# Kernel tuning notes

Measured on AMD Instinct MI355X. Metric: run time of the kernel, lower is better.

## Reference

```python
import jax, jax.numpy as jnp
import numpy as np

QMAX = 32767.0   # 2**15 - 1
QMIN = -32768.0  # -2**15


def setup_inputs() -> dict:
    key = jax.random.key(0)
    k_x, k_w0, k_w1, k_s, k_b = jax.random.split(key, 5)
    N, Cin, Cout = 8192, 4096, 4096
    x = jax.random.normal(k_x, (N, Cin, 1, 1), dtype=jnp.float32)
    # Fake-quantized INT8 weights: build a fp32 weight, split into dual int8 planes
    # the same way prepare_from_weight does, so w0/w1 hold integer values in [-128,127].
    W = jax.random.normal(k_w0, (Cout, Cin), dtype=jnp.float32) * 0.02
    max_abs = jnp.maximum(jnp.max(jnp.abs(W), axis=1), 1e-8)
    s0 = max_abs / 127.0
    w0 = jnp.clip(jnp.round(W / s0[:, None]), -128.0, 127.0)
    R = W - s0[:, None] * w0
    max_abs_R = jnp.max(jnp.abs(R), axis=1)
    s1 = jnp.where(max_abs_R > 1e-3, max_abs_R / 127.0, 0.0)
    w1 = jnp.where((s1 > 0)[:, None],
                   jnp.clip(jnp.round(R / jnp.where(s1 > 0, s1, 1.0)[:, None]), -128.0, 127.0),
                   0.0)
    bias = jax.random.normal(k_b, (Cout,), dtype=jnp.float32) * 0.01
    return {"x": x, "w0": w0, "w1": w1, "s0": s0, "s1": s1, "bias": bias}


def reference(x, w0, w1, s0, s1, bias):
    N, Cin, H, W_ = x.shape  # H == W_ == 1
    x2d = x.reshape(N, Cin)
    # INT16 activation fake-quant with softplus-smoothed amax
    amax = jnp.max(jnp.abs(x2d), axis=1, keepdims=True)          # [N,1]
    scale_x = jax.nn.softplus(amax) / QMAX                       # [N,1]
    xq = jnp.clip(jnp.round(x2d / scale_x), QMIN, QMAX)          # [N,Cin]
    # dual 1x1 convs == two GEMMs: [N,Cin] x [Cin,Cout]
    y0 = jnp.einsum('nc,oc->no', xq, w0)
    y1 = jnp.einsum('nc,oc->no', xq, w1)
    y = (y0 * s0[None, :] + y1 * s1[None, :]) * scale_x + bias[None, :]
    return y.reshape(N, -1, 1, 1)
```

## Files before the change

### kernel.cpp

```cpp
#include <hip/hip_runtime.h>
#include <hip/hip_fp16.h>

#define N_ROWS 8192
#define K_DIM  4096
#define M_DIM  4096

typedef __attribute__((ext_vector_type(8))) _Float16 half8;
typedef __attribute__((ext_vector_type(4))) _Float16 half4v;
typedef __attribute__((ext_vector_type(4))) float    f32x4;

__global__ __launch_bounds__(256) void prologue_kernel(
    const float* __restrict__ x,  _Float16* __restrict__ xq, float* __restrict__ sx,
    const float* __restrict__ w0, const float* __restrict__ w1,
    const float* __restrict__ s0, const float* __restrict__ s1,
    _Float16* __restrict__ wp)
{
    const int t = threadIdx.x;
    if (blockIdx.x < N_ROWS) {
        const int row = blockIdx.x;
        const float4* xr4 = (const float4*)(x + (size_t)row * K_DIM);

        float4 v[4];
        float am = 0.0f;
#pragma unroll
        for (int i = 0; i < 4; ++i) {
            v[i] = xr4[i * 256 + t];
            am = fmaxf(am, fmaxf(fmaxf(fabsf(v[i].x), fabsf(v[i].y)),
                                 fmaxf(fabsf(v[i].z), fabsf(v[i].w))));
        }
#pragma unroll
        for (int off = 32; off; off >>= 1)
            am = fmaxf(am, __shfl_xor(am, off, 64));
        __shared__ float red[4];
        if ((t & 63) == 0) red[t >> 6] = am;
        __syncthreads();
        am = fmaxf(fmaxf(red[0], red[1]), fmaxf(red[2], red[3]));

        const float sp    = (am > 20.0f) ? am : log1pf(expf(am));
        const float scale = sp / 32767.0f;
        const float inv   = 32767.0f / sp;
        if (t == 0) sx[row] = scale;

        half4v* out4 = (half4v*)(xq + (size_t)row * K_DIM);
#pragma unroll
        for (int i = 0; i < 4; ++i) {
            float q0 = fminf(fmaxf(rintf(v[i].x * inv), -32768.0f), 32767.0f);
            float q1 = fminf(fmaxf(rintf(v[i].y * inv), -32768.0f), 32767.0f);
            float q2 = fminf(fmaxf(rintf(v[i].z * inv), -32768.0f), 32767.0f);
            float q3 = fminf(fmaxf(rintf(v[i].w * inv), -32768.0f), 32767.0f);
            half4v h;
            h[0] = (_Float16)q0; h[1] = (_Float16)q1;
            h[2] = (_Float16)q2; h[3] = (_Float16)q3;
            out4[i * 256 + t] = h;
        }
    } else {
        const size_t gid  = (size_t)(blockIdx.x - N_ROWS) * 256 + t;
        const size_t base = gid * 8;
        const int    o    = (int)(base >> 12);
        const float  a = s0[o], b = s1[o];

        const float4* p0 = (const float4*)(w0 + base);
        const float4* p1 = (const float4*)(w1 + base);
        float4 u0 = p0[0], u1 = p0[1];
        float4 v0 = p1[0], v1 = p1[1];

        half8 h;
        h[0] = (_Float16)(a * u0.x + b * v0.x);
        h[1] = (_Float16)(a * u0.y + b * v0.y);
        h[2] = (_Float16)(a * u0.z + b * v0.z);
        h[3] = (_Float16)(a * u0.w + b * v0.w);
        h[4] = (_Float16)(a * u1.x + b * v1.x);
        h[5] = (_Float16)(a * u1.y + b * v1.y);
        h[6] = (_Float16)(a * u1.z + b * v1.z);
        h[7] = (_Float16)(a * u1.w + b * v1.w);
        *(half8*)(wp + base) = h;
    }
}

__device__ inline void async_load16(const void* g, void* l)
{
    __builtin_amdgcn_global_load_lds(
        (const __attribute__((address_space(1))) void*)g,
        (__attribute__((address_space(3))) void*)l, 16, 0, 0);
}

__global__ __launch_bounds__(256) void gemm_kernel(
    const _Float16* __restrict__ A,
    const _Float16* __restrict__ B,
    const float* __restrict__ sx,
    const float* __restrict__ bias,
    float* __restrict__ out)
{
    __shared__ __align__(16) _Float16 As[128 * 32];
    __shared__ __align__(16) _Float16 Bs[128 * 32];

    const int t    = threadIdx.x;
    const int wave = t >> 6;
    const int lane = t & 63;

    const int tile = blockIdx.x >> 6;
    const int loc  = blockIdx.x & 63;
    const int o0   = ((tile & 3) * 8 + (loc & 7)) * 128;
    const int n0   = ((tile >> 2) * 8 + (loc >> 3)) * 128;

    const int srow = lane >> 2;
    const int scl  = lane & 3;
    const int scg  = scl ^ ((srow >> 1) & 3);
    const int gcol = scg * 8;
    const int lcol = scl * 8;

    const int n_off = (wave >> 1) * 64;
    const int o_off = (wave & 1) * 64;

    const int fr = lane & 15;
    const int fg = lane >> 4;
    const int fk = (fg ^ ((fr >> 1) & 3)) * 8;

    f32x4 acc[4][4] = {};

    for (int kk = 0; kk < K_DIM; kk += 32) {
#pragma unroll
        for (int j = 0; j < 2; ++j) {
            const int row = j * 64 + wave * 16 + srow;
            async_load16(A + (size_t)(n0 + row) * K_DIM + kk + gcol,
                         &As[row * 32 + lcol]);
            async_load16(B + (size_t)(o0 + row) * K_DIM + kk + gcol,
                         &Bs[row * 32 + lcol]);
        }
        __syncthreads();

        half8 af[4], bf[4];
#pragma unroll
        for (int i = 0; i < 4; ++i)
            af[i] = *(const half8*)&As[(n_off + i * 16 + fr) * 32 + fk];
#pragma unroll
        for (int j = 0; j < 4; ++j)
            bf[j] = *(const half8*)&Bs[(o_off + j * 16 + fr) * 32 + fk];

#pragma unroll
        for (int i = 0; i < 4; ++i)
#pragma unroll
            for (int j = 0; j < 4; ++j)
                acc[i][j] = __builtin_amdgcn_mfma_f32_16x16x32_f16(
                    af[i], bf[j], acc[i][j], 0, 0, 0);

        __syncthreads();
    }

#pragma unroll
    for (int i = 0; i < 4; ++i) {
        const int nbase = n0 + n_off + i * 16 + (lane >> 4) * 4;
#pragma unroll
        for (int r = 0; r < 4; ++r) {
            const float s = sx[nbase + r];
            float* orow = out + (size_t)(nbase + r) * M_DIM;
#pragma unroll
            for (int j = 0; j < 4; ++j) {
                const int o = o0 + o_off + j * 16 + (lane & 15);
                orow[o] = acc[i][j][r] * s + bias[o];
            }
        }
    }
}

extern "C" void kernel_launch(void* const* d_in, const int* in_sizes, int n_in,
                              void* d_out, int out_size, void* d_ws, size_t ws_size,
                              hipStream_t stream)
{
    const float* x    = (const float*)d_in[0];
    const float* w0   = (const float*)d_in[1];
    const float* w1   = (const float*)d_in[2];
    const float* s0   = (const float*)d_in[3];
    const float* s1   = (const float*)d_in[4];
    const float* bias = (const float*)d_in[5];
    float* out = (float*)d_out;

    char* ws = (char*)d_ws;
    _Float16* xq = (_Float16*)ws;
    _Float16* wp = (_Float16*)(ws + (size_t)N_ROWS * K_DIM * 2);
    float*    sx = (float*)(ws + (size_t)N_ROWS * K_DIM * 2
                               + (size_t)M_DIM * K_DIM * 2);

    prologue_kernel<<<N_ROWS + (M_DIM * K_DIM) / (256 * 8), 256, 0, stream>>>(
        x, xq, sx, w0, w1, s0, s1, wp);

    gemm_kernel<<<(N_ROWS / 128) * (M_DIM / 128), 256, 0, stream>>>(
        xq, wp, sx, bias, out);
}
```

Measured before the change: 638.8 us.

## Rewrite GEMM as 256x256 double-buffered pipelined kernel with wave-per-row prologue

The GEMM moves from 128x128 tiles with K=32 steps and a full sync per step to 256x256 tiles with 512 threads and K=64 double-buffered LDS stages. Async global-to-LDS loads are issued per quarter-phase, interleaved with MFMA work, and gated by explicit vmcnt waits and s_setprio. The block order is swizzled for L2 reuse and bias is loaded once into registers. The prologue now processes one activation row per wave, removing the LDS reduction and block barrier, and handles 16 weights per thread. This targets load latency and barrier stalls, at the cost of much higher register and LDS pressure (128 KB LDS per block) and delicate wait-count correctness.

Result: faster. 605.7 us (-5.2%).

```diff
diff --git a/kernel.cpp b/kernel.cpp
--- a/kernel.cpp
+++ b/kernel.cpp
@@ -4,6 +4,8 @@
 #define N_ROWS 8192
 #define K_DIM  4096
 #define M_DIM  4096
+#define NT     (K_DIM / 64)
+#define HT_MAX (4 * NT)
 
 typedef __attribute__((ext_vector_type(8))) _Float16 half8;
 typedef __attribute__((ext_vector_type(4))) _Float16 half4v;
@@ -16,64 +18,63 @@
     _Float16* __restrict__ wp)
 {
     const int t = threadIdx.x;
-    if (blockIdx.x < N_ROWS) {
-        const int row = blockIdx.x;
+    if (blockIdx.x < N_ROWS / 4) {
+        const int lane = t & 63;
+        const int row  = blockIdx.x * 4 + (t >> 6);
         const float4* xr4 = (const float4*)(x + (size_t)row * K_DIM);
 
-        float4 v[4];
+        float4 v[16];
         float am = 0.0f;
 #pragma unroll
-        for (int i = 0; i < 4; ++i) {
-            v[i] = xr4[i * 256 + t];
-            am = fmaxf(am, fmaxf(fmaxf(fabsf(v[i].x), fabsf(v[i].y)),
-                                 fmaxf(fabsf(v[i].z), fabsf(v[i].w))));
+        for (int j = 0; j < 16; ++j) {
+            v[j] = xr4[j * 64 + lane];
+            am = fmaxf(am, fmaxf(fmaxf(fabsf(v[j].x), fabsf(v[j].y)),
+                                 fmaxf(fabsf(v[j].z), fabsf(v[j].w))));
         }
 #pragma unroll
         for (int off = 32; off; off >>= 1)
             am = fmaxf(am, __shfl_xor(am, off, 64));
-        __shared__ float red[4];
-        if ((t & 63) == 0) red[t >> 6] = am;
-        __syncthreads();
-        am = fmaxf(fmaxf(red[0], red[1]), fmaxf(red[2], red[3]));
 
         const float sp    = (am > 20.0f) ? am : log1pf(expf(am));
-        const float scale = sp / 32767.0f;
+        const float scale = sp * (1.0f / 32767.0f);
         const float inv   = 32767.0f / sp;
-        if (t == 0) sx[row] = scale;
+        if (lane == 0) sx[row] = scale;
 
         half4v* out4 = (half4v*)(xq + (size_t)row * K_DIM);
 #pragma unroll
-        for (int i = 0; i < 4; ++i) {
-            float q0 = fminf(fmaxf(rintf(v[i].x * inv), -32768.0f), 32767.0f);
-            float q1 = fminf(fmaxf(rintf(v[i].y * inv), -32768.0f), 32767.0f);
-            float q2 = fminf(fmaxf(rintf(v[i].z * inv), -32768.0f), 32767.0f);
-            float q3 = fminf(fmaxf(rintf(v[i].w * inv), -32768.0f), 32767.0f);
+        for (int j = 0; j < 16; ++j) {
             half4v h;
-            h[0] = (_Float16)q0; h[1] = (_Float16)q1;
-            h[2] = (_Float16)q2; h[3] = (_Float16)q3;
-            out4[i * 256 + t] = h;
+            h[0] = (_Float16)fminf(fmaxf(rintf(v[j].x * inv), -32768.0f), 32767.0f);
+            h[1] = (_Float16)fminf(fmaxf(rintf(v[j].y * inv), -32768.0f), 32767.0f);
+            h[2] = (_Float16)fminf(fmaxf(rintf(v[j].z * inv), -32768.0f), 32767.0f);
+            h[3] = (_Float16)fminf(fmaxf(rintf(v[j].w * inv), -32768.0f), 32767.0f);
+            out4[j * 64 + lane] = h;
         }
     } else {
-        const size_t gid  = (size_t)(blockIdx.x - N_ROWS) * 256 + t;
-        const size_t base = gid * 8;
+        const size_t gid  = (size_t)(blockIdx.x - N_ROWS / 4) * 256 + t;
+        const size_t base = gid * 16;
         const int    o    = (int)(base >> 12);
         const float  a = s0[o], b = s1[o];
 
         const float4* p0 = (const float4*)(w0 + base);
         const float4* p1 = (const float4*)(w1 + base);
-        float4 u0 = p0[0], u1 = p0[1];
-        float4 v0 = p1[0], v1 = p1[1];
-
-        half8 h;
-        h[0] = (_Float16)(a * u0.x + b * v0.x);
-        h[1] = (_Float16)(a * u0.y + b * v0.y);
-        h[2] = (_Float16)(a * u0.z + b * v0.z);
-        h[3] = (_Float16)(a * u0.w + b * v0.w);
-        h[4] = (_Float16)(a * u1.x + b * v1.x);
-        h[5] = (_Float16)(a * u1.y + b * v1.y);
-        h[6] = (_Float16)(a * u1.z + b * v1.z);
-        h[7] = (_Float16)(a * u1.w + b * v1.w);
-        *(half8*)(wp + base) = h;
+        float4 u[4], w[4];
+#pragma unroll
+        for (int j = 0; j < 4; ++j) { u[j] = p0[j]; w[j] = p1[j]; }
+
+#pragma unroll
+        for (int hv = 0; hv < 2; ++hv) {
+            half8 h;
+#pragma unroll
+            for (int j = 0; j < 2; ++j) {
+                const float4 uu = u[hv * 2 + j], ww = w[hv * 2 + j];
+                h[j * 4 + 0] = (_Float16)(a * uu.x + b * ww.x);
+                h[j * 4 + 1] = (_Float16)(a * uu.y + b * ww.y);
+                h[j * 4 + 2] = (_Float16)(a * uu.z + b * ww.z);
+                h[j * 4 + 3] = (_Float16)(a * uu.w + b * ww.w);
+            }
+            *(half8*)(wp + base + hv * 8) = h;
+        }
     }
 }
 
@@ -84,81 +85,138 @@
         (__attribute__((address_space(3))) void*)l, 16, 0, 0);
 }
 
-__global__ __launch_bounds__(256) void gemm_kernel(
+#define PHASE(BUF, QM, QN, HT, GATE)                                          \
+    {                                                                         \
+        half8 af[4][2], bf[2][2];                                             \
+        _Pragma("unroll")                                                     \
+        for (int i = 0; i < 4; ++i) {                                         \
+            const int r = wm * 128 + (QM) * 64 + i * 16 + fr;                 \
+            _Pragma("unroll")                                                 \
+            for (int ks = 0; ks < 2; ++ks) {                                  \
+                const int c = (ks * 4 + fg) ^ (r & 7);                        \
+                af[i][ks] = *(const half8*)&As[BUF][r * 64 + c * 8];          \
+            }                                                                 \
+        }                                                                     \
+        _Pragma("unroll")                                                     \
+        for (int j = 0; j < 2; ++j) {                                         \
+            const int r = wn * 64 + (QN) * 32 + j * 16 + fr;                  \
+            _Pragma("unroll")                                                 \
+            for (int ks = 0; ks < 2; ++ks) {                                  \
+                const int c = (ks * 4 + fg) ^ (r & 7);                        \
+                bf[j][ks] = *(const half8*)&Bs[BUF][r * 64 + c * 8];          \
+            }                                                                 \
+        }                                                                     \
+        stage(HT);                                                            \
+        __builtin_amdgcn_s_barrier();                                         \
+        asm volatile("" ::: "memory");                                        \
+        asm volatile("s_waitcnt lgkmcnt(0)" ::: "memory");                    \
+        __builtin_amdgcn_sched_barrier(0);                                    \
+        __builtin_amdgcn_s_setprio(1);                                        \
+        _Pragma("unroll")                                                     \
+        for (int ks = 0; ks < 2; ++ks)                                        \
+            _Pragma("unroll")                                                 \
+            for (int i = 0; i < 4; ++i)                                       \
+                _Pragma("unroll")                                             \
+                for (int j = 0; j < 2; ++j)                                   \
+                    acc[(QM) * 4 + i][(QN) * 2 + j] =                         \
+                        __builtin_amdgcn_mfma_f32_16x16x32_f16(               \
+                            af[i][ks], bf[j][ks],                             \
+                            acc[(QM) * 4 + i][(QN) * 2 + j], 0, 0, 0);        \
+        __builtin_amdgcn_s_setprio(0);                                        \
+        if ((GATE) == 0)                                                      \
+            asm volatile("s_waitcnt vmcnt(0)" ::: "memory");                  \
+        else if ((GATE) > 0)                                                  \
+            asm volatile("s_waitcnt vmcnt(4)" ::: "memory");                  \
+        __builtin_amdgcn_s_barrier();                                         \
+        asm volatile("" ::: "memory");                                        \
+    }
+
+__global__ __launch_bounds__(512, 2) void gemm_kernel(
     const _Float16* __restrict__ A,
     const _Float16* __restrict__ B,
     const float* __restrict__ sx,
     const float* __restrict__ bias,
     float* __restrict__ out)
 {
-    __shared__ __align__(16) _Float16 As[128 * 32];
-    __shared__ __align__(16) _Float16 Bs[128 * 32];
+    __shared__ __align__(16) _Float16 As[2][256 * 64];
+    __shared__ __align__(16) _Float16 Bs[2][256 * 64];
 
     const int t    = threadIdx.x;
+    const int lane = t & 63;
     const int wave = t >> 6;
-    const int lane = t & 63;
-
-    const int tile = blockIdx.x >> 6;
-    const int loc  = blockIdx.x & 63;
-    const int o0   = ((tile & 3) * 8 + (loc & 7)) * 128;
-    const int n0   = ((tile >> 2) * 8 + (loc >> 3)) * 128;
-
-    const int srow = lane >> 2;
-    const int scl  = lane & 3;
-    const int scg  = scl ^ ((srow >> 1) & 3);
-    const int gcol = scg * 8;
-    const int lcol = scl * 8;
-
-    const int n_off = (wave >> 1) * 64;
-    const int o_off = (wave & 1) * 64;
+    const int wm   = wave >> 2;
+    const int wn   = wave & 3;
+
+    const int b2  = (blockIdx.x & 7) * 64 + (blockIdx.x >> 3);
+    const int sup = b2 >> 6;
+    const int loc = b2 & 63;
+    const int tm  = (sup & 1) * 8 + (loc & 7);
+    const int tn  = (sup >> 1) * 8 + (loc >> 3);
+    const int n0  = tn * 256;
+    const int o0  = tm * 256;
 
     const int fr = lane & 15;
     const int fg = lane >> 4;
-    const int fk = (fg ^ ((fr >> 1) & 3)) * 8;
-
-    f32x4 acc[4][4] = {};
-
-    for (int kk = 0; kk < K_DIM; kk += 32) {
-#pragma unroll
-        for (int j = 0; j < 2; ++j) {
-            const int row = j * 64 + wave * 16 + srow;
-            async_load16(A + (size_t)(n0 + row) * K_DIM + kk + gcol,
-                         &As[row * 32 + lcol]);
-            async_load16(B + (size_t)(o0 + row) * K_DIM + kk + gcol,
-                         &Bs[row * 32 + lcol]);
-        }
-        __syncthreads();
-
-        half8 af[4], bf[4];
-#pragma unroll
-        for (int i = 0; i < 4; ++i)
-            af[i] = *(const half8*)&As[(n_off + i * 16 + fr) * 32 + fk];
-#pragma unroll
-        for (int j = 0; j < 4; ++j)
-            bf[j] = *(const half8*)&Bs[(o_off + j * 16 + fr) * 32 + fk];
-
-#pragma unroll
-        for (int i = 0; i < 4; ++i)
+
+    f32x4 acc[8][4] = {};
+
+    auto stage = [&](int ht_) {
+        if (ht_ >= HT_MAX) return;
+        const int Tt  = ht_ >> 2;
+        const int prt = ht_ & 3;
+        const int kof = Tt * 64;
+        _Float16* lbase = (prt & 1) ? &Bs[Tt & 1][0] : &As[Tt & 1][0];
+        const _Float16* gbase = (prt & 1) ? B + (size_t)o0 * K_DIM
+                                          : A + (size_t)n0 * K_DIM;
+#pragma unroll
+        for (int l = 0; l < 2; ++l) {
+            const int s  = l * 512 + t;
+            const int hr = s >> 3;
+            const int pc = s & 7;
+            int r;
+            if (prt & 1) r = ((hr >> 5) << 6) | ((prt & 2) ? 32 : 0) | (hr & 31);
+            else         r = ((hr >> 6) << 7) | ((prt & 2) ? 64 : 0) | (hr & 63);
+            const int c = pc ^ (r & 7);
+            async_load16(gbase + (size_t)r * K_DIM + kof + c * 8,
+                         lbase + r * 64 + pc * 8);
+        }
+    };
+
+#pragma unroll
+    for (int h = 0; h < 6; ++h) stage(h);
+    asm volatile("s_waitcnt vmcnt(4)" ::: "memory");
+    __builtin_amdgcn_s_barrier();
+    asm volatile("" ::: "memory");
+
+    int ht = 6;
+#pragma unroll 1
+    for (int it = 0; it < NT / 2; ++it) {
+        const int g = (it == NT / 2 - 1) ? 0 : 4;
+        PHASE(0, 0, 0, ht + 0, -1)
+        PHASE(0, 0, 1, ht + 1, -1)
+        PHASE(0, 1, 0, ht + 2, -1)
+        PHASE(0, 1, 1, ht + 3, g)
+        PHASE(1, 0, 0, ht + 4, -1)
+        PHASE(1, 0, 1, ht + 5, -1)
+        PHASE(1, 1, 0, ht + 6, -1)
+        PHASE(1, 1, 1, ht + 7, g)
+        ht += 8;
+    }
+
+    float bs[4];
+#pragma unroll
+    for (int j = 0; j < 4; ++j)
+        bs[j] = bias[o0 + wn * 64 + j * 16 + fr];
+#pragma unroll
+    for (int i = 0; i < 8; ++i) {
+        const int nb = n0 + wm * 128 + i * 16 + fg * 4;
+#pragma unroll
+        for (int r = 0; r < 4; ++r) {
+            const float s = sx[nb + r];
+            float* orow = out + (size_t)(nb + r) * M_DIM;
 #pragma unroll
             for (int j = 0; j < 4; ++j)
-                acc[i][j] = __builtin_amdgcn_mfma_f32_16x16x32_f16(
-                    af[i], bf[j], acc[i][j], 0, 0, 0);
-
-        __syncthreads();
-    }
-
-#pragma unroll
-    for (int i = 0; i < 4; ++i) {
-        const int nbase = n0 + n_off + i * 16 + (lane >> 4) * 4;
-#pragma unroll
-        for (int r = 0; r < 4; ++r) {
-            const float s = sx[nbase + r];
-            float* orow = out + (size_t)(nbase + r) * M_DIM;
-#pragma unroll
-            for (int j = 0; j < 4; ++j) {
-                const int o = o0 + o_off + j * 16 + (lane & 15);
-                orow[o] = acc[i][j][r] * s + bias[o];
-            }
+                orow[o0 + wn * 64 + j * 16 + fr] = acc[i][j][r] * s + bs[j];
         }
     }
 }
@@ -181,9 +239,9 @@
     float*    sx = (float*)(ws + (size_t)N_ROWS * K_DIM * 2
                                + (size_t)M_DIM * K_DIM * 2);
 
-    prologue_kernel<<<N_ROWS + (M_DIM * K_DIM) / (256 * 8), 256, 0, stream>>>(
+    prologue_kernel<<<N_ROWS / 4 + (M_DIM * K_DIM) / (256 * 16), 256, 0, stream>>>(
         x, xq, sx, w0, w1, s0, s1, wp);
 
-    gemm_kernel<<<(N_ROWS / 128) * (M_DIM / 128), 256, 0, stream>>>(
+    gemm_kernel<<<(N_ROWS / 256) * (M_DIM / 256), 512, 0, stream>>>(
         xq, wp, sx, bias, out);
 }
```
